# Optimization experiments

Measured on AMD Instinct MI355X. Metric: run time of the kernel, lower is better.

## Reference

```python
import jax, jax.numpy as jnp
import numpy as np
from jax import lax

DIM = 1024
B, N = 4, 4096


def setup_inputs() -> dict:
    key = jax.random.key(0)
    k1, k2 = jax.random.split(key)
    x = jax.random.normal(k1, (B, N, DIM), dtype=jnp.float32)
    # Linear(dim, 3*dim, bias=False): weight stored as [3*dim, dim] (torch convention)
    w_qkva = jax.random.normal(k2, (3 * DIM, DIM), dtype=jnp.float32) * (DIM ** -0.5)
    gamma = jnp.ones((DIM,), dtype=jnp.float32)  # RMSNorm gain
    return {"x": x, "w_qkva": w_qkva, "gamma": gamma}


def _rmsnorm(x, gamma):
    # lucidrains RMSNorm: F.normalize(x, dim=-1) * sqrt(dim) * gamma
    scale = jnp.asarray(x.shape[-1], x.dtype) ** 0.5
    norm = jnp.sqrt(jnp.sum(x * x, axis=-1, keepdims=True))
    return x / jnp.maximum(norm, 1e-12) * scale * gamma


def reference(x, w_qkva, gamma):
    h = _rmsnorm(x, gamma)                                  # [b, n, d]
    qkva = jnp.einsum('bnd,ed->bne', h, w_qkva)             # [b, n, 3d]
    q, kv, a = jnp.split(qkva, 3, axis=-1)                  # each [b, n, d]
    a = jax.nn.sigmoid(a)

    def binary_operator(e_i, e_j):
        a_i, kv_i = e_i
        a_j, kv_j = e_j
        return (a_j * a_i, a_j * kv_i + kv_j)

    # gated linear recurrence over the sequence axis (elementwise per channel)
    _, y = lax.associative_scan(binary_operator, (a, kv), axis=1)
    return q * y                                            # [b, n, d]
```

## Files before the change

### kernel.cpp

```cpp
#include <hip/hip_runtime.h>
#include <hip/hip_bf16.h>

#define SEQ_N 4096
#define BATCH 4
#define DIM 1024
#define M_ROWS (BATCH * SEQ_N)
#define NCOLS (3 * DIM)
#define KDIM DIM
#define CHUNK_L 32
#define NCHUNK (SEQ_N / CHUNK_L)
#define NCHANNEL (BATCH * DIM)

using short8 = __attribute__((ext_vector_type(8))) short;
using f32x4  = __attribute__((ext_vector_type(4))) float;

static __device__ __forceinline__ unsigned short f2bf(float f) {
    union { float f; unsigned u; } v; v.f = f;
    unsigned r = v.u + 0x7fffu + ((v.u >> 16) & 1u);
    return (unsigned short)(r >> 16);
}
static __device__ __forceinline__ float bf2f(unsigned short s) {
    union { unsigned u; float f; } v; v.u = ((unsigned)s) << 16;
    return v.f;
}
static __device__ __forceinline__ float sigm(float x) {
    return 1.f / (1.f + __expf(-x));
}

__global__ __launch_bounds__(256) void wconv_kernel(const float* __restrict__ in,
                                                    unsigned short* __restrict__ out,
                                                    int n4) {
    int i = blockIdx.x * 256 + threadIdx.x;
    if (i < n4) {
        float4 v = reinterpret_cast<const float4*>(in)[i];
        ushort4 o;
        o.x = f2bf(v.x); o.y = f2bf(v.y); o.z = f2bf(v.z); o.w = f2bf(v.w);
        reinterpret_cast<ushort4*>(out)[i] = o;
    }
}

__global__ __launch_bounds__(256) void rmsnorm_kernel(const float* __restrict__ x,
                                                      const float* __restrict__ gamma,
                                                      unsigned short* __restrict__ h) {
    const int row = blockIdx.x;
    const int tid = threadIdx.x;
    const float4 v = reinterpret_cast<const float4*>(x + (size_t)row * DIM)[tid];
    float ss = v.x * v.x + v.y * v.y + v.z * v.z + v.w * v.w;
#pragma unroll
    for (int off = 32; off >= 1; off >>= 1) ss += __shfl_xor(ss, off, 64);
    __shared__ float red[4];
    if ((tid & 63) == 0) red[tid >> 6] = ss;
    __syncthreads();
    const float tot = red[0] + red[1] + red[2] + red[3];
    const float scale = 32.0f / fmaxf(sqrtf(tot), 1e-12f);
    const float4 g = reinterpret_cast<const float4*>(gamma)[tid];
    ushort4 o;
    o.x = f2bf(v.x * scale * g.x);
    o.y = f2bf(v.y * scale * g.y);
    o.z = f2bf(v.z * scale * g.z);
    o.w = f2bf(v.w * scale * g.w);
    reinterpret_cast<ushort4*>(h + (size_t)row * DIM)[tid] = o;
}

__global__ __launch_bounds__(256) void gemm_bt_kernel(const unsigned short* __restrict__ A,
                                                      const unsigned short* __restrict__ B,
                                                      unsigned short* __restrict__ C) {
    __shared__ __align__(16) unsigned short sA[128 * 32];
    __shared__ __align__(16) unsigned short sB[128 * 32];

    const int tid  = threadIdx.x;
    const int lane = tid & 63;
    const int wave = tid >> 6;
    const int row0 = blockIdx.y * 128;
    const int col0 = blockIdx.x * 128;
    const int wm = (wave >> 1) * 64;
    const int wn = (wave & 1) * 64;
    const int fr = lane & 15;
    const int kq = lane >> 4;

    const unsigned short* agp = A + (size_t)(row0 + (tid >> 2)) * KDIM + (tid & 3) * 8;
    const unsigned short* bgp = B + (size_t)(col0 + (tid >> 2)) * KDIM + (tid & 3) * 8;

    f32x4 acc[4][4] = {};

    for (int k0 = 0; k0 < KDIM; k0 += 32) {
        __builtin_amdgcn_global_load_lds(
            (const __attribute__((address_space(1))) void*)(agp),
            (__attribute__((address_space(3))) void*)(&sA[tid * 8]), 16, 0, 0);
        __builtin_amdgcn_global_load_lds(
            (const __attribute__((address_space(1))) void*)(agp + 64 * KDIM),
            (__attribute__((address_space(3))) void*)(&sA[2048 + tid * 8]), 16, 0, 0);
        __builtin_amdgcn_global_load_lds(
            (const __attribute__((address_space(1))) void*)(bgp),
            (__attribute__((address_space(3))) void*)(&sB[tid * 8]), 16, 0, 0);
        __builtin_amdgcn_global_load_lds(
            (const __attribute__((address_space(1))) void*)(bgp + 64 * KDIM),
            (__attribute__((address_space(3))) void*)(&sB[2048 + tid * 8]), 16, 0, 0);
        agp += 32; bgp += 32;
        __syncthreads();

        short8 af[4], bf[4];
#pragma unroll
        for (int i = 0; i < 4; ++i)
            af[i] = *reinterpret_cast<const short8*>(&sA[(wm + i * 16 + fr) * 32 + kq * 8]);
#pragma unroll
        for (int j = 0; j < 4; ++j)
            bf[j] = *reinterpret_cast<const short8*>(&sB[(wn + j * 16 + fr) * 32 + kq * 8]);
#pragma unroll
        for (int i = 0; i < 4; ++i)
#pragma unroll
            for (int j = 0; j < 4; ++j)
                acc[i][j] = __builtin_amdgcn_mfma_f32_16x16x32_bf16(af[i], bf[j], acc[i][j], 0, 0, 0);
        __syncthreads();
    }

#pragma unroll
    for (int i = 0; i < 4; ++i) {
#pragma unroll
        for (int j = 0; j < 4; ++j) {
#pragma unroll
            for (int r = 0; r < 4; ++r) {
                int row = row0 + wm + i * 16 + kq * 4 + r;
                int col = col0 + wn + j * 16 + fr;
                C[(size_t)row * NCOLS + col] = f2bf(acc[i][j][r]);
            }
        }
    }
}

__global__ __launch_bounds__(256) void chunk_agg_kernel(const unsigned short* __restrict__ qkva,
                                                        float* __restrict__ Aagg,
                                                        float* __restrict__ Yagg) {
    const int c = blockIdx.x, b = blockIdx.y;
    const int d4 = threadIdx.x * 4;
    const unsigned short* base = qkva + ((size_t)b * SEQ_N + c * CHUNK_L) * NCOLS;
    float s[4] = {0.f, 0.f, 0.f, 0.f};
    float A[4] = {1.f, 1.f, 1.f, 1.f};
#pragma unroll 4
    for (int n = 0; n < CHUNK_L; ++n) {
        const ushort4 kvu = *reinterpret_cast<const ushort4*>(base + (size_t)n * NCOLS + DIM + d4);
        const ushort4 au  = *reinterpret_cast<const ushort4*>(base + (size_t)n * NCOLS + 2 * DIM + d4);
        const float kv[4] = {bf2f(kvu.x), bf2f(kvu.y), bf2f(kvu.z), bf2f(kvu.w)};
        const float av[4] = {bf2f(au.x),  bf2f(au.y),  bf2f(au.z),  bf2f(au.w)};
#pragma unroll
        for (int j = 0; j < 4; ++j) {
            const float a = sigm(av[j]);
            s[j] = fmaf(a, s[j], kv[j]);
            A[j] *= a;
        }
    }
    const int idx = c * NCHANNEL + b * DIM + d4;
    float4 Ao, Yo;
    Ao.x = A[0]; Ao.y = A[1]; Ao.z = A[2]; Ao.w = A[3];
    Yo.x = s[0]; Yo.y = s[1]; Yo.z = s[2]; Yo.w = s[3];
    *reinterpret_cast<float4*>(&Aagg[idx]) = Ao;
    *reinterpret_cast<float4*>(&Yagg[idx]) = Yo;
}

__global__ __launch_bounds__(256) void agg_scan_kernel(const float* __restrict__ Aagg,
                                                       const float* __restrict__ Yagg,
                                                       float* __restrict__ Sin) {
    const int ch = blockIdx.x * 256 + threadIdx.x;
    float s = 0.f;
#pragma unroll 8
    for (int c = 0; c < NCHUNK; ++c) {
        const float A = Aagg[c * NCHANNEL + ch];
        const float Y = Yagg[c * NCHANNEL + ch];
        Sin[c * NCHANNEL + ch] = s;
        s = fmaf(A, s, Y);
    }
}

__global__ __launch_bounds__(256) void apply_kernel(const unsigned short* __restrict__ qkva,
                                                    const float* __restrict__ Sin,
                                                    float* __restrict__ out) {
    const int c = blockIdx.x, b = blockIdx.y;
    const int d4 = threadIdx.x * 4;
    const unsigned short* base = qkva + ((size_t)b * SEQ_N + c * CHUNK_L) * NCOLS;
    float* obase = out + ((size_t)b * SEQ_N + c * CHUNK_L) * DIM;
    const float4 s0 = *reinterpret_cast<const float4*>(&Sin[c * NCHANNEL + b * DIM + d4]);
    float s[4] = {s0.x, s0.y, s0.z, s0.w};
#pragma unroll 2
    for (int n = 0; n < CHUNK_L; ++n) {
        const ushort4 qu  = *reinterpret_cast<const ushort4*>(base + (size_t)n * NCOLS + d4);
        const ushort4 kvu = *reinterpret_cast<const ushort4*>(base + (size_t)n * NCOLS + DIM + d4);
        const ushort4 au  = *reinterpret_cast<const ushort4*>(base + (size_t)n * NCOLS + 2 * DIM + d4);
        const float kv[4] = {bf2f(kvu.x), bf2f(kvu.y), bf2f(kvu.z), bf2f(kvu.w)};
        const float av[4] = {bf2f(au.x),  bf2f(au.y),  bf2f(au.z),  bf2f(au.w)};
        const float q[4]  = {bf2f(qu.x),  bf2f(qu.y),  bf2f(qu.z),  bf2f(qu.w)};
        float4 o;
#pragma unroll
        for (int j = 0; j < 4; ++j) {
            const float a = sigm(av[j]);
            s[j] = fmaf(a, s[j], kv[j]);
        }
        o.x = q[0] * s[0]; o.y = q[1] * s[1]; o.z = q[2] * s[2]; o.w = q[3] * s[3];
        *reinterpret_cast<float4*>(&obase[(size_t)n * DIM + d4]) = o;
    }
}

extern "C" void kernel_launch(void* const* d_in, const int* in_sizes, int n_in,
                              void* d_out, int out_size, void* d_ws, size_t ws_size,
                              hipStream_t stream) {
    const float* x     = (const float*)d_in[0];
    const float* w     = (const float*)d_in[1];
    const float* gamma = (const float*)d_in[2];
    float* out = (float*)d_out;

    char* ws = (char*)d_ws;
    unsigned short* wb   = (unsigned short*)(ws);
    unsigned short* h    = (unsigned short*)(ws + 6291456);
    unsigned short* qkva = (unsigned short*)(ws + 39845888);
    float* Aagg = (float*)(ws + 6291456);
    float* Yagg = (float*)(ws + 6291456 + 2097152);
    float* Sin  = (float*)(ws + 6291456 + 4194304);

    wconv_kernel<<<(NCOLS * KDIM / 4 + 255) / 256, 256, 0, stream>>>(w, wb, NCOLS * KDIM / 4);
    rmsnorm_kernel<<<M_ROWS, 256, 0, stream>>>(x, gamma, h);
    gemm_bt_kernel<<<dim3(NCOLS / 128, M_ROWS / 128), 256, 0, stream>>>(h, wb, qkva);
    chunk_agg_kernel<<<dim3(NCHUNK, BATCH), 256, 0, stream>>>(qkva, Aagg, Yagg);
    agg_scan_kernel<<<NCHANNEL / 256, 256, 0, stream>>>(Aagg, Yagg, Sin);
    apply_kernel<<<dim3(NCHUNK, BATCH), 256, 0, stream>>>(qkva, Sin, out);
}
```

Baseline: 299.1 us.

## Rewrite QKVA GEMM as 256x256 tiles with 4-stage LDS pipeline and swizzle

Replaces the 128x128 single-buffered GEMM with a 512-thread kernel that computes 256x256 output tiles. It uses a 4-buffer LDS ring with global_load_lds prefetch two k-steps ahead, interleaves the loads with MFMA phases under s_setprio, and remaps block indices so consecutive blocks share A/B tiles in L2. The goal is to hide global load latency, remove the per-iteration full syncs, and raise arithmetic intensity. The cost is 64KB of LDS and heavy register pressure from 32 accumulators per thread, and the hand-placed waitcnt/barrier ordering is fragile.

```diff
diff --git a/kernel.cpp b/kernel.cpp
--- a/kernel.cpp
+++ b/kernel.cpp
@@ -10,6 +10,7 @@
 #define CHUNK_L 32
 #define NCHUNK (SEQ_N / CHUNK_L)
 #define NCHANNEL (BATCH * DIM)
+#define GT 32
 
 using short8 = __attribute__((ext_vector_type(8))) short;
 using f32x4  = __attribute__((ext_vector_type(4))) float;
@@ -62,60 +63,104 @@
     reinterpret_cast<ushort4*>(h + (size_t)row * DIM)[tid] = o;
 }
 
-__global__ __launch_bounds__(256) void gemm_bt_kernel(const unsigned short* __restrict__ A,
-                                                      const unsigned short* __restrict__ B,
-                                                      unsigned short* __restrict__ C) {
-    __shared__ __align__(16) unsigned short sA[128 * 32];
-    __shared__ __align__(16) unsigned short sB[128 * 32];
+__global__ __launch_bounds__(512, 2) void gemm256_kernel(const unsigned short* __restrict__ A,
+                                                         const unsigned short* __restrict__ B,
+                                                         unsigned short* __restrict__ C) {
+    __shared__ __align__(16) unsigned short sA[4][256][32];
+    __shared__ __align__(16) unsigned short sB[4][256][32];
 
     const int tid  = threadIdx.x;
     const int lane = tid & 63;
     const int wave = tid >> 6;
-    const int row0 = blockIdx.y * 128;
-    const int col0 = blockIdx.x * 128;
-    const int wm = (wave >> 1) * 64;
-    const int wn = (wave & 1) * 64;
+
+    const int orig = blockIdx.x;
+    const int swz  = (orig & 7) * 96 + (orig >> 3);
+    const int ntile = swz >> 6;
+    const int mtile = swz & 63;
+    const int row0 = mtile * 256;
+    const int col0 = ntile * 256;
+
+    const int wm = (wave >> 2) * 128;
+    const int wn = (wave & 3) * 64;
     const int fr = lane & 15;
     const int kq = lane >> 4;
 
-    const unsigned short* agp = A + (size_t)(row0 + (tid >> 2)) * KDIM + (tid & 3) * 8;
-    const unsigned short* bgp = B + (size_t)(col0 + (tid >> 2)) * KDIM + (tid & 3) * 8;
-
-    f32x4 acc[4][4] = {};
-
-    for (int k0 = 0; k0 < KDIM; k0 += 32) {
-        __builtin_amdgcn_global_load_lds(
-            (const __attribute__((address_space(1))) void*)(agp),
-            (__attribute__((address_space(3))) void*)(&sA[tid * 8]), 16, 0, 0);
-        __builtin_amdgcn_global_load_lds(
-            (const __attribute__((address_space(1))) void*)(agp + 64 * KDIM),
-            (__attribute__((address_space(3))) void*)(&sA[2048 + tid * 8]), 16, 0, 0);
-        __builtin_amdgcn_global_load_lds(
-            (const __attribute__((address_space(1))) void*)(bgp),
-            (__attribute__((address_space(3))) void*)(&sB[tid * 8]), 16, 0, 0);
-        __builtin_amdgcn_global_load_lds(
-            (const __attribute__((address_space(1))) void*)(bgp + 64 * KDIM),
-            (__attribute__((address_space(3))) void*)(&sB[2048 + tid * 8]), 16, 0, 0);
-        agp += 32; bgp += 32;
-        __syncthreads();
-
-        short8 af[4], bf[4];
-#pragma unroll
-        for (int i = 0; i < 4; ++i)
-            af[i] = *reinterpret_cast<const short8*>(&sA[(wm + i * 16 + fr) * 32 + kq * 8]);
+    const int srow = tid >> 2;
+    const int scol = (tid & 3) * 8;
+    const unsigned short* aSrc = A + (size_t)(row0 + srow) * KDIM + scol;
+    const unsigned short* bSrc = B + (size_t)(col0 + srow) * KDIM + scol;
+    unsigned short* sAf = &sA[0][0][0];
+    unsigned short* sBf = &sB[0][0][0];
+    const int sdst = tid * 8;
+
+#define STAGE_A(bs, kt, u)                                                              \
+    __builtin_amdgcn_global_load_lds(                                                   \
+        (const __attribute__((address_space(1))) void*)(aSrc + (size_t)(u) * 128 * KDIM + (kt) * 32), \
+        (__attribute__((address_space(3))) void*)(sAf + (bs) * 8192 + (u) * 4096 + sdst), 16, 0, 0);
+#define STAGE_B(bs, kt, u)                                                              \
+    __builtin_amdgcn_global_load_lds(                                                   \
+        (const __attribute__((address_space(1))) void*)(bSrc + (size_t)(u) * 128 * KDIM + (kt) * 32), \
+        (__attribute__((address_space(3))) void*)(sBf + (bs) * 8192 + (u) * 4096 + sdst), 16, 0, 0);
+
+    f32x4 acc[8][4] = {};
+
+    STAGE_A(0, 0, 0); STAGE_A(0, 0, 1); STAGE_B(0, 0, 0); STAGE_B(0, 0, 1);
+    STAGE_A(1, 1, 0); STAGE_A(1, 1, 1); STAGE_B(1, 1, 0); STAGE_B(1, 1, 1);
+    asm volatile("s_waitcnt vmcnt(4)" ::: "memory");
+    __builtin_amdgcn_sched_barrier(0);
+    __builtin_amdgcn_s_barrier();
+
+    for (int t = 0; t < GT; ++t) {
+        const int b  = t & 3;
+        const int bs = (t + 2) & 3;
+        const bool st = (t + 2 < GT);
+        const unsigned short* sAb = sAf + b * 8192;
+        const unsigned short* sBb = sBf + b * 8192;
+
+        short8 bfr[4], afr[4];
 #pragma unroll
         for (int j = 0; j < 4; ++j)
-            bf[j] = *reinterpret_cast<const short8*>(&sB[(wn + j * 16 + fr) * 32 + kq * 8]);
+            bfr[j] = *reinterpret_cast<const short8*>(sBb + (wn + j * 16 + fr) * 32 + kq * 8);
+#pragma unroll
+        for (int i = 0; i < 4; ++i)
+            afr[i] = *reinterpret_cast<const short8*>(sAb + (wm + i * 16 + fr) * 32 + kq * 8);
+        if (st) { STAGE_A(bs, t + 2, 0); STAGE_A(bs, t + 2, 1); }
+        __builtin_amdgcn_s_barrier();
+        __builtin_amdgcn_s_setprio(1);
 #pragma unroll
         for (int i = 0; i < 4; ++i)
 #pragma unroll
             for (int j = 0; j < 4; ++j)
-                acc[i][j] = __builtin_amdgcn_mfma_f32_16x16x32_bf16(af[i], bf[j], acc[i][j], 0, 0, 0);
-        __syncthreads();
-    }
-
-#pragma unroll
-    for (int i = 0; i < 4; ++i) {
+                acc[i][j] = __builtin_amdgcn_mfma_f32_16x16x32_bf16(afr[i], bfr[j], acc[i][j], 0, 0, 0);
+        __builtin_amdgcn_s_setprio(0);
+        __builtin_amdgcn_s_barrier();
+
+        short8 afr2[4];
+#pragma unroll
+        for (int i = 0; i < 4; ++i)
+            afr2[i] = *reinterpret_cast<const short8*>(sAb + (wm + 64 + i * 16 + fr) * 32 + kq * 8);
+        if (st) { STAGE_B(bs, t + 2, 0); STAGE_B(bs, t + 2, 1); }
+        __builtin_amdgcn_s_barrier();
+        __builtin_amdgcn_s_setprio(1);
+#pragma unroll
+        for (int i = 0; i < 4; ++i)
+#pragma unroll
+            for (int j = 0; j < 4; ++j)
+                acc[4 + i][j] = __builtin_amdgcn_mfma_f32_16x16x32_bf16(afr2[i], bfr[j], acc[4 + i][j], 0, 0, 0);
+        __builtin_amdgcn_s_setprio(0);
+        if (t < GT - 2) {
+            asm volatile("s_waitcnt vmcnt(4)" ::: "memory");
+        } else if (t == GT - 2) {
+            asm volatile("s_waitcnt vmcnt(0)" ::: "memory");
+        }
+        __builtin_amdgcn_sched_barrier(0);
+        __builtin_amdgcn_s_barrier();
+    }
+#undef STAGE_A
+#undef STAGE_B
+
+#pragma unroll
+    for (int i = 0; i < 8; ++i) {
 #pragma unroll
         for (int j = 0; j < 4; ++j) {
 #pragma unroll
@@ -217,7 +262,7 @@
 
     wconv_kernel<<<(NCOLS * KDIM / 4 + 255) / 256, 256, 0, stream>>>(w, wb, NCOLS * KDIM / 4);
     rmsnorm_kernel<<<M_ROWS, 256, 0, stream>>>(x, gamma, h);
-    gemm_bt_kernel<<<dim3(NCOLS / 128, M_ROWS / 128), 256, 0, stream>>>(h, wb, qkva);
+    gemm256_kernel<<<(M_ROWS / 256) * (NCOLS / 256), 512, 0, stream>>>(h, wb, qkva);
     chunk_agg_kernel<<<dim3(NCHUNK, BATCH), 256, 0, stream>>>(qkva, Aagg, Yagg);
     agg_scan_kernel<<<NCHANNEL / 256, 256, 0, stream>>>(Aagg, Yagg, Sin);
     apply_kernel<<<dim3(NCHUNK, BATCH), 256, 0, stream>>>(qkva, Sin, out);
```

Result: no change. 296.9 us (-0.7%).
